# Kernel optimization log

Hardware: AMD Instinct MI355X
Metric: run time of the kernel (lower is better)

## Reference

```python
import jax, jax.numpy as jnp
import numpy as np

B, T, D, S, ITERS = 32, 4096, 256, 8, 3
SCALE = D ** -0.5
EPS = 1e-8


def _ln(x, g, b):
    mu = jnp.mean(x, axis=-1, keepdims=True)
    var = jnp.var(x, axis=-1, keepdims=True)
    return (x - mu) / jnp.sqrt(var + 1e-5) * g + b


def setup_inputs() -> dict:
    key = jax.random.key(0)
    ks = jax.random.split(key, 16)
    w = lambda k, shp, s=0.02: jax.random.normal(k, shp, jnp.float32) * s
    return {
        "inputs": jax.random.normal(ks[0], (B, T, D), jnp.float32),
        "slots_mu": w(ks[1], (1, 1, D), 0.1),
        "slots_logsigma": w(ks[2], (1, 1, D), 0.1),
        "noise": jax.random.normal(ks[3], (B, S, D), jnp.float32),
        "Wq": w(ks[4], (D, D)),
        "Wk": w(ks[5], (D, D)),
        "Wv": w(ks[6], (D, D)),
        "norm_g": jnp.ones((D,), jnp.float32),
        "norm_b": jnp.zeros((D,), jnp.float32),
        "gru_wih": w(ks[7], (D, 3 * D)),
        "gru_whh": w(ks[8], (D, 3 * D)),
        "gru_bih": jnp.zeros((3 * D,), jnp.float32),
        "gru_bhh": jnp.zeros((3 * D,), jnp.float32),
        "mlp_ng": jnp.ones((D,), jnp.float32),
        "mlp_nb": jnp.zeros((D,), jnp.float32),
        "mlp_w1": w(ks[9], (D, 4 * D)),
        "mlp_b1": jnp.zeros((4 * D,), jnp.float32),
        "mlp_w2": w(ks[10], (4 * D, D)),
        "mlp_b2": jnp.zeros((D,), jnp.float32),
    }


def reference(inputs, slots_mu, slots_logsigma, noise, Wq, Wk, Wv, norm_g, norm_b,
              gru_wih, gru_whh, gru_bih, gru_bhh, mlp_ng, mlp_nb,
              mlp_w1, mlp_b1, mlp_w2, mlp_b2):
    # init slots: mu + sigma * noise, broadcast [1,1,D] -> [B,S,D]
    slots = slots_mu + jnp.exp(slots_logsigma) * noise

    keys = inputs @ Wk      # [B,T,D]
    values = inputs @ Wv    # [B,T,D]

    for _ in range(ITERS):
        slots_prev = slots
        s_n = _ln(slots, norm_g, norm_b)
        q = s_n @ Wq                                    # [B,S,D]
        dots = jnp.einsum('bsd,btd->bst', q, keys) * SCALE
        attn = jax.nn.softmax(dots, axis=1) + EPS       # softmax over slots
        attn = attn / jnp.sum(attn, axis=-1, keepdims=True)
        updates = jnp.einsum('bst,btd->bsd', attn, values)

        # GRUCell: x = updates, h = slots_prev (elementwise over B*S)
        gi = updates @ gru_wih + gru_bih                # [B,S,3D]
        gh = slots_prev @ gru_whh + gru_bhh
        ir, iz, inn = jnp.split(gi, 3, axis=-1)
        hr, hz, hn = jnp.split(gh, 3, axis=-1)
        r = jax.nn.sigmoid(ir + hr)
        z = jax.nn.sigmoid(iz + hz)
        n = jnp.tanh(inn + r * hn)
        slots = (1.0 - z) * n + z * slots_prev

        # pre-norm residual MLP
        h = _ln(slots, mlp_ng, mlp_nb)
        h = jax.nn.relu(h @ mlp_w1 + mlp_b1)
        slots = slots + (h @ mlp_w2 + mlp_b2)

    return slots
```

## Files before the change

### kernel.cpp

```cpp
#include <hip/hip_runtime.h>
#include <stdint.h>

#define B_ 32
#define T_ 4096
#define D_ 256
#define S_ 8
#define ITERS_ 3
#define SCALE_ 0.0625f
#define EPS_ 1e-8f
#define NCH 16
#define CHUNK (T_/NCH)

typedef short short8 __attribute__((ext_vector_type(8)));
typedef float f32x4 __attribute__((ext_vector_type(4)));

__device__ __forceinline__ uint32_t f2bf1(float x){
  union { float f; uint32_t u; } c; c.f = x;
  return (c.u + 0x7fffu + ((c.u >> 16) & 1u)) >> 16;
}
__device__ __forceinline__ uint32_t pack2bf(float a, float b){
  return f2bf1(a) | (f2bf1(b) << 16);
}
__device__ __forceinline__ uint32_t cvtpk2bf(float a, float b){
  uint32_t r;
  asm("v_cvt_pk_bf16_f32 %0, %1, %2" : "=v"(r) : "v"(a), "v"(b));
  return r;
}
__device__ __forceinline__ float bflo(uint32_t u){ union{uint32_t u;float f;} c; c.u = u << 16; return c.f; }
__device__ __forceinline__ float bfhi(uint32_t u){ union{uint32_t u;float f;} c; c.u = u & 0xffff0000u; return c.f; }

__global__ __launch_bounds__(256) void k_prep(const float* __restrict__ Wk, const float* __restrict__ Wv,
                                              const float* __restrict__ Wq,
                                              const float* __restrict__ wih, const float* __restrict__ whh,
                                              const float* __restrict__ bih, const float* __restrict__ bhh,
                                              const float* __restrict__ w1, const float* __restrict__ w2,
                                              const float* __restrict__ mu, const float* __restrict__ ls,
                                              const float* __restrict__ noise,
                                              uint16_t* __restrict__ Wt, uint16_t* __restrict__ Wqt,
                                              uint16_t* __restrict__ Bcat, float* __restrict__ bc,
                                              uint16_t* __restrict__ w1t, uint16_t* __restrict__ w2t,
                                              float* __restrict__ slots){
  int g = blockIdx.x, tid = threadIdx.x;
  if (g < 512){
    int n = g, k = tid;
    float v = (n < 256) ? Wk[k*256 + n] : Wv[k*256 + (n - 256)];
    Wt[n*256 + k] = (uint16_t)f2bf1(v);
  } else if (g < 768){
    int n = g - 512, k = tid;
    Wqt[n*256 + k] = (uint16_t)f2bf1(Wq[k*256 + n] * SCALE_);
  } else if (g < 1792){
    int n = g - 768;
    #pragma unroll
    for (int j = 0; j < 2; ++j){
      int k = j*256 + tid;
      float v;
      if (n < 768) v = (k < 256) ? wih[k*768 + n] : whh[(k-256)*768 + n];
      else         v = (k < 256) ? 0.f            : whh[(k-256)*768 + 512 + (n-768)];
      Bcat[(size_t)n*512 + k] = (uint16_t)f2bf1(v);
    }
  } else if (g < 1793){
    #pragma unroll
    for (int j = 0; j < 4; ++j){
      int i = j*256 + tid;
      float v;
      if (i < 512) v = bih[i] + bhh[i];
      else if (i < 768) v = bih[i];
      else v = bhh[i - 256];
      bc[i] = v;
    }
  } else if (g < 2817){
    int n = g - 1793, k = tid;
    w1t[(size_t)n*256 + k] = (uint16_t)f2bf1(w1[(size_t)k*1024 + n]);
  } else if (g < 3073){
    int n = g - 2817;
    #pragma unroll
    for (int j = 0; j < 4; ++j){
      int k = j*256 + tid;
      w2t[(size_t)n*1024 + k] = (uint16_t)f2bf1(w2[(size_t)k*256 + n]);
    }
  } else {
    int i = (g - 3073)*256 + tid;
    int d = i & 255;
    slots[i] = mu[d] + __expf(ls[d]) * noise[i];
  }
}

#define PPITCH 40
__global__ __launch_bounds__(256) void k_proj(const float* __restrict__ X,
                                              const uint16_t* __restrict__ Wt,
                                              uint16_t* __restrict__ Kp,
                                              uint16_t* __restrict__ Vp){
  __shared__ __align__(16) uint16_t As[128*PPITCH];
  __shared__ __align__(16) uint16_t Bs[128*PPITCH];
  __shared__ __align__(16) uint16_t Cs[128*128];
  int bid = blockIdx.x;
  int x = bid & 7, j = bid >> 3;
  int tau = 512*x + j;
  int mt = tau >> 2;
  int nt = tau & 3;
  int m0 = mt * 128;
  int n0 = nt * 128;
  int tid = threadIdx.x;
  int lane = tid & 63, wid = tid >> 6;
  int wm = wid >> 1, wn = wid & 1;
  int rsel = lane & 15, g = lane >> 4;

  f32x4 acc[4][4];
  for (int a = 0; a < 4; ++a)
    for (int b = 0; b < 4; ++b)
      acc[a][b] = (f32x4){0.f,0.f,0.f,0.f};

  for (int ks = 0; ks < 8; ++ks){
    int k0 = ks*32;
    #pragma unroll
    for (int i = 0; i < 2; ++i){
      int task = i*256 + tid;
      int row = task >> 2, seg = task & 3;
      const float* gp = X + (size_t)(m0 + row)*256 + k0 + seg*8;
      float4 a = *(const float4*)gp;
      float4 b = *(const float4*)(gp + 4);
      uint4 w;
      w.x = cvtpk2bf(a.x, a.y); w.y = cvtpk2bf(a.z, a.w);
      w.z = cvtpk2bf(b.x, b.y); w.w = cvtpk2bf(b.z, b.w);
      *(uint4*)&As[row*PPITCH + seg*8] = w;
    }
    #pragma unroll
    for (int i = 0; i < 2; ++i){
      int task = i*256 + tid;
      int row = task >> 2, seg = task & 3;
      uint4 v = *(const uint4*)(Wt + (size_t)(n0 + row)*256 + k0 + seg*8);
      *(uint4*)&Bs[row*PPITCH + seg*8] = v;
    }
    __syncthreads();
    short8 af[4], bfr[4];
    #pragma unroll
    for (int t = 0; t < 4; ++t)
      af[t] = *(const short8*)&As[(wm*64 + t*16 + rsel)*PPITCH + g*8];
    #pragma unroll
    for (int t = 0; t < 4; ++t)
      bfr[t] = *(const short8*)&Bs[(wn*64 + t*16 + rsel)*PPITCH + g*8];
    #pragma unroll
    for (int a = 0; a < 4; ++a)
      #pragma unroll
      for (int b = 0; b < 4; ++b)
        acc[a][b] = __builtin_amdgcn_mfma_f32_16x16x32_bf16(af[a], bfr[b], acc[a][b], 0, 0, 0);
    __syncthreads();
  }
  #pragma unroll
  for (int a = 0; a < 4; ++a)
    #pragma unroll
    for (int b = 0; b < 4; ++b)
      #pragma unroll
      for (int r = 0; r < 4; ++r){
        int mrow = wm*64 + a*16 + g*4 + r;
        int ncol = wn*64 + b*16 + rsel;
        Cs[mrow*128 + ncol] = (uint16_t)f2bf1(acc[a][b][r]);
      }
  __syncthreads();
  uint16_t* outp = (n0 < 256) ? Kp : Vp;
  int nbase = n0 & 255;
  #pragma unroll
  for (int i = 0; i < 4; ++i){
    int task = i*256 + tid;
    int row = task >> 3, seg = task & 7;
    uint4 v = *(uint4*)&Cs[row*128 + seg*16];
    *(uint4*)&outp[(size_t)(m0 + row)*256 + nbase + seg*16] = v;
  }
}

__global__ __launch_bounds__(256) void k_qln(const float* __restrict__ slots,
                                             const uint16_t* __restrict__ Wqt,
                                             const float* __restrict__ ng,
                                             const float* __restrict__ nb,
                                             uint16_t* __restrict__ qbf){
  __shared__ __align__(16) uint16_t snl[16*264];
  int m0 = blockIdx.x * 16;
  int tid = threadIdx.x;
  int r = tid >> 4, cs = (tid & 15) * 16;
  float xv[16];
  {
    const float* sp = slots + (size_t)(m0 + r)*256 + cs;
    #pragma unroll
    for (int i = 0; i < 4; ++i){
      float4 v = *(const float4*)(sp + i*4);
      xv[i*4+0]=v.x; xv[i*4+1]=v.y; xv[i*4+2]=v.z; xv[i*4+3]=v.w;
    }
  }
  float s1 = 0.f, s2 = 0.f;
  #pragma unroll
  for (int i = 0; i < 16; ++i){ s1 += xv[i]; s2 += xv[i]*xv[i]; }
  #pragma unroll
  for (int m = 1; m < 16; m <<= 1){ s1 += __shfl_xor(s1, m, 64); s2 += __shfl_xor(s2, m, 64); }
  float mu = s1 * (1.f/256.f);
  float ms = s2 * (1.f/256.f);
  float rstd = rsqrtf(ms - mu*mu + 1e-5f);
  {
    uint32_t pk[8];
    #pragma unroll
    for (int i = 0; i < 8; ++i){
      float a = (xv[2*i]   - mu)*rstd*ng[cs+2*i]   + nb[cs+2*i];
      float b = (xv[2*i+1] - mu)*rstd*ng[cs+2*i+1] + nb[cs+2*i+1];
      pk[i] = pack2bf(a, b);
    }
    uint4* dst = (uint4*)&snl[r*264 + cs];
    dst[0] = (uint4){pk[0],pk[1],pk[2],pk[3]};
    dst[1] = (uint4){pk[4],pk[5],pk[6],pk[7]};
  }
  __syncthreads();
  int lane = tid & 63, w = tid >> 6;
  int rsel = lane & 15, g = lane >> 4;
  short8 aq[8];
  #pragma unroll
  for (int kk = 0; kk < 8; ++kk)
    aq[kk] = *(const short8*)((const char*)snl + rsel*528 + kk*64 + g*16);
  int n0w = w*64;
  #pragma unroll
  for (int nt = 0; nt < 4; ++nt){
    f32x4 acc = (f32x4){0.f,0.f,0.f,0.f};
    #pragma unroll
    for (int kk = 0; kk < 8; ++kk){
      short8 bfr = *(const short8*)&Wqt[(size_t)(n0w + nt*16 + rsel)*256 + kk*32 + g*8];
      acc = __builtin_amdgcn_mfma_f32_16x16x32_bf16(aq[kk], bfr, acc, 0, 0, 0);
    }
    #pragma unroll
    for (int r4 = 0; r4 < 4; ++r4){
      int row = g*4 + r4;
      qbf[(size_t)(m0 + row)*256 + n0w + nt*16 + rsel] = (uint16_t)f2bf1(acc[r4]);
    }
  }
}

#define GPIT 40
__global__ __launch_bounds__(256) void k_gemmG(const uint16_t* __restrict__ A,
                                               const uint16_t* __restrict__ Bm,
                                               float* __restrict__ Cf){
  __shared__ __align__(16) uint16_t As[64*GPIT];
  __shared__ __align__(16) uint16_t Bs[64*GPIT];
  const int N = 1024, K = 512;
  int m0 = blockIdx.y * 64, n0 = blockIdx.x * 64;
  int tid = threadIdx.x, lane = tid & 63, wid = tid >> 6;
  int wm = wid >> 1, wn = wid & 1;
  int rsel = lane & 15, g = lane >> 4;
  f32x4 acc[2][2];
  #pragma unroll
  for (int a = 0; a < 2; ++a)
    #pragma unroll
    for (int b = 0; b < 2; ++b)
      acc[a][b] = (f32x4){0.f,0.f,0.f,0.f};
  int row_s = tid >> 2, seg = tid & 3;
  for (int k0 = 0; k0 < K; k0 += 32){
    *(uint4*)&As[row_s*GPIT + seg*8] = *(const uint4*)(A  + (size_t)(m0+row_s)*K + k0 + seg*8);
    *(uint4*)&Bs[row_s*GPIT + seg*8] = *(const uint4*)(Bm + (size_t)(n0+row_s)*K + k0 + seg*8);
    __syncthreads();
    short8 af[2], bfr[2];
    #pragma unroll
    for (int t = 0; t < 2; ++t)
      af[t]  = *(const short8*)&As[(wm*32 + t*16 + rsel)*GPIT + g*8];
    #pragma unroll
    for (int t = 0; t < 2; ++t)
      bfr[t] = *(const short8*)&Bs[(wn*32 + t*16 + rsel)*GPIT + g*8];
    #pragma unroll
    for (int a = 0; a < 2; ++a)
      #pragma unroll
      for (int b = 0; b < 2; ++b)
        acc[a][b] = __builtin_amdgcn_mfma_f32_16x16x32_bf16(af[a], bfr[b], acc[a][b], 0, 0, 0);
    __syncthreads();
  }
  #pragma unroll
  for (int a = 0; a < 2; ++a)
    #pragma unroll
    for (int b = 0; b < 2; ++b)
      #pragma unroll
      for (int r = 0; r < 4; ++r){
        int mrow = m0 + wm*32 + a*16 + g*4 + r;
        int ncol = n0 + wn*32 + b*16 + rsel;
        Cf[(size_t)mrow*N + ncol] = acc[a][b][r];
      }
}

__global__ __launch_bounds__(256) void k_gru_pre(const float* __restrict__ upd_part,
                                                 const float* __restrict__ sum_part,
                                                 const float* __restrict__ slots,
                                                 uint16_t* __restrict__ Acat){
  int row = blockIdx.x;
  int b = row >> 3, s = row & 7;
  int d = threadIdx.x;
  float sum = 0.f;
  #pragma unroll
  for (int ch = 0; ch < 16; ++ch) sum += sum_part[(size_t)(b*16 + ch)*8 + s];
  float acc = 0.f;
  #pragma unroll
  for (int ch = 0; ch < 16; ++ch) acc += upd_part[(size_t)(b*16 + ch)*2048 + s*256 + d];
  Acat[(size_t)row*512 + d]       = (uint16_t)f2bf1(acc / sum);
  Acat[(size_t)row*512 + 256 + d] = (uint16_t)f2bf1(slots[row*256 + d]);
}

__global__ __launch_bounds__(256) void k_combine(const float* __restrict__ G,
                                                 const float* __restrict__ bc,
                                                 const float* __restrict__ slots,
                                                 const float* __restrict__ mng,
                                                 const float* __restrict__ mnb,
                                                 float* __restrict__ s2f,
                                                 uint16_t* __restrict__ snb){
  __shared__ float red[8];
  int row = blockIdx.x, c = threadIdx.x;
  int lane = c & 63, wid = c >> 6;
  const float* Gr = G + (size_t)row*1024;
  float r  = 1.f / (1.f + __expf(-(Gr[c]       + bc[c])));
  float z  = 1.f / (1.f + __expf(-(Gr[256 + c] + bc[256 + c])));
  float Gn = Gr[512 + c], Gh = Gr[768 + c];
  float nn = tanhf((Gn - Gh + bc[512 + c]) + r*(Gh + bc[768 + c]));
  float hv = slots[row*256 + c];
  float s2 = (1.f - z)*nn + z*hv;
  s2f[row*256 + c] = s2;
  float p1 = s2, p2 = s2*s2;
  #pragma unroll
  for (int d = 32; d; d >>= 1){ p1 += __shfl_down(p1, d, 64); p2 += __shfl_down(p2, d, 64); }
  if (lane == 0){ red[wid] = p1; red[4 + wid] = p2; }
  __syncthreads();
  float mu = (red[0]+red[1]+red[2]+red[3]) * (1.f/256.f);
  float ms = (red[4]+red[5]+red[6]+red[7]) * (1.f/256.f);
  float rstd = rsqrtf(ms - mu*mu + 1e-5f);
  snb[row*256 + c] = (uint16_t)f2bf1((s2 - mu)*rstd*mng[c] + mnb[c]);
}

#define HPIT 1048
__global__ __launch_bounds__(256) void k_mlp(const uint16_t* __restrict__ snb,
                                             const uint16_t* __restrict__ w1t,
                                             const float* __restrict__ b1,
                                             const uint16_t* __restrict__ w2t,
                                             const float* __restrict__ b2,
                                             const float* __restrict__ s2f,
                                             float* __restrict__ slots){
  __shared__ __align__(16) uint16_t h1s[16*HPIT];
  int m0 = blockIdx.x * 16;
  int tid = threadIdx.x, lane = tid & 63, w = tid >> 6;
  int rsel = lane & 15, g = lane >> 4;
  short8 aq[8];
  #pragma unroll
  for (int kk = 0; kk < 8; ++kk)
    aq[kk] = *(const short8*)&snb[(size_t)(m0 + rsel)*256 + kk*32 + g*8];
  #pragma unroll
  for (int nt = 0; nt < 16; ++nt){
    int ncol = w*256 + nt*16 + rsel;
    f32x4 acc = (f32x4){0.f,0.f,0.f,0.f};
    #pragma unroll
    for (int kk = 0; kk < 8; ++kk){
      short8 bfr = *(const short8*)&w1t[(size_t)ncol*256 + kk*32 + g*8];
      acc = __builtin_amdgcn_mfma_f32_16x16x32_bf16(aq[kk], bfr, acc, 0, 0, 0);
    }
    float bv = b1[ncol];
    #pragma unroll
    for (int r4 = 0; r4 < 4; ++r4){
      int row = g*4 + r4;
      h1s[row*HPIT + ncol] = (uint16_t)f2bf1(fmaxf(acc[r4] + bv, 0.f));
    }
  }
  __syncthreads();
  f32x4 acc2[4];
  #pragma unroll
  for (int nt = 0; nt < 4; ++nt) acc2[nt] = (f32x4){0.f,0.f,0.f,0.f};
  for (int kk = 0; kk < 32; ++kk){
    short8 aq2 = *(const short8*)((const char*)h1s + rsel*2096 + kk*64 + g*16);
    #pragma unroll
    for (int nt = 0; nt < 4; ++nt){
      short8 bfr = *(const short8*)&w2t[(size_t)(w*64 + nt*16 + rsel)*1024 + kk*32 + g*8];
      acc2[nt] = __builtin_amdgcn_mfma_f32_16x16x32_bf16(aq2, bfr, acc2[nt], 0, 0, 0);
    }
  }
  #pragma unroll
  for (int nt = 0; nt < 4; ++nt){
    int ncol = w*64 + nt*16 + rsel;
    float bv = b2[ncol];
    #pragma unroll
    for (int r4 = 0; r4 < 4; ++r4){
      int row = m0 + g*4 + r4;
      slots[(size_t)row*256 + ncol] = s2f[(size_t)row*256 + ncol] + acc2[nt][r4] + bv;
    }
  }
}

__global__ __launch_bounds__(256) void k_attn(const uint16_t* __restrict__ qbf,
                                              const uint16_t* __restrict__ Kp,
                                              const uint16_t* __restrict__ Vp,
                                              float* __restrict__ upd_part,
                                              float* __restrict__ sum_part){
  __shared__ __align__(16) uint16_t qs[16*264];
  __shared__ __align__(16) uint16_t Ks[64*264];
  __shared__ __align__(16) uint32_t attp[64*4];
  __shared__ float red[8*256];
  __shared__ float ssum[8];
  int bid = blockIdx.x;
  int b = bid >> 4, ch = bid & 15;
  int tid = threadIdx.x, lane = tid & 63, wid = tid >> 6;
  {
    const uint32_t* qg = (const uint32_t*)(qbf + (size_t)b*2048);
    uint32_t* qd = (uint32_t*)qs;
    #pragma unroll
    for (int i = 0; i < 4; ++i){
      int idx = i*256 + tid;
      int s = idx >> 7, c = idx & 127;
      qd[s*132 + c] = qg[idx];
    }
    #pragma unroll
    for (int i = 0; i < 5; ++i){
      int idx = i*256 + tid;
      if (idx < 1056) qd[8*132 + idx] = 0u;
    }
  }
  if (tid < 8) ssum[tid] = 0.f;
  __syncthreads();
  short8 aq[8];
  {
    int rs = lane & 15, g = lane >> 4;
    const char* qb = (const char*)qs;
    #pragma unroll
    for (int kk = 0; kk < 8; ++kk)
      aq[kk] = *(const short8*)(qb + rs*528 + kk*64 + g*16);
  }
  float upd[8][4];
  #pragma unroll
  for (int s = 0; s < 8; ++s){ upd[s][0]=0.f; upd[s][1]=0.f; upd[s][2]=0.f; upd[s][3]=0.f; }
  float sp[4] = {0.f,0.f,0.f,0.f};
  int dd = lane * 4;
  int tq = wid;

  for (int st = 0; st < 4; ++st){
    int t0 = ch*CHUNK + st*64;
    {
      const char* kg = (const char*)Kp + ((size_t)(b*T_ + t0) << 9);
      char* kd = (char*)Ks;
      #pragma unroll
      for (int i = 0; i < 8; ++i){
        int task = i*256 + tid;
        int row = task >> 5, seg = task & 31;
        uint4 v = *(const uint4*)(kg + (row << 9) + (seg << 4));
        *(uint4*)(kd + row*528 + seg*16) = v;
      }
    }
    __syncthreads();
    f32x4 dot = (f32x4){0.f,0.f,0.f,0.f};
    int col = lane & 15, g = lane >> 4;
    {
      const char* kb = (const char*)Ks + (wid*16 + col)*528 + g*16;
      #pragma unroll
      for (int kk = 0; kk < 8; ++kk){
        short8 bf = *(const short8*)(kb + kk*64);
        dot = __builtin_amdgcn_mfma_f32_16x16x32_bf16(aq[kk], bf, dot, 0, 0, 0);
      }
    }
    float x0 = dot[0], x1 = dot[1], x2 = dot[2], x3 = dot[3];
    float y0 = __shfl_xor(x0, 16, 64), y1 = __shfl_xor(x1, 16, 64);
    float y2 = __shfl_xor(x2, 16, 64), y3 = __shfl_xor(x3, 16, 64);
    float m = fmaxf(fmaxf(fmaxf(x0,x1), fmaxf(x2,x3)), fmaxf(fmaxf(y0,y1), fmaxf(y2,y3)));
    float e0 = __expf(x0-m), e1 = __expf(x1-m), e2 = __expf(x2-m), e3 = __expf(x3-m);
    float f0 = __expf(y0-m), f1 = __expf(y1-m), f2 = __expf(y2-m), f3 = __expf(y3-m);
    float inv = 1.f / (e0+e1+e2+e3+f0+f1+f2+f3);
    float p0 = e0*inv + EPS_, p1 = e1*inv + EPS_, p2 = e2*inv + EPS_, p3 = e3*inv + EPS_;
    if (g < 2){
      sp[0] += p0; sp[1] += p1; sp[2] += p2; sp[3] += p3;
      int t = wid*16 + col;
      attp[t*4 + g*2 + 0] = pack2bf(p0, p1);
      attp[t*4 + g*2 + 1] = pack2bf(p2, p3);
    }
    __syncthreads();
    {
      const char* vg = (const char*)Vp + ((size_t)(b*T_ + t0) << 9) + (size_t)dd*2;
      #pragma unroll
      for (int tt = 0; tt < 16; ++tt){
        int tl = tq*16 + tt;
        uint2 vv = *(const uint2*)(vg + ((size_t)tl << 9));
        uint4 aa = *(const uint4*)&attp[tl*4];
        float v0 = bflo(vv.x), v1 = bfhi(vv.x), v2 = bflo(vv.y), v3 = bfhi(vv.y);
        float av[8];
        av[0] = bflo(aa.x); av[1] = bfhi(aa.x); av[2] = bflo(aa.y); av[3] = bfhi(aa.y);
        av[4] = bflo(aa.z); av[5] = bfhi(aa.z); av[6] = bflo(aa.w); av[7] = bfhi(aa.w);
        #pragma unroll
        for (int s = 0; s < 8; ++s){
          upd[s][0] = fmaf(av[s], v0, upd[s][0]);
          upd[s][1] = fmaf(av[s], v1, upd[s][1]);
          upd[s][2] = fmaf(av[s], v2, upd[s][2]);
          upd[s][3] = fmaf(av[s], v3, upd[s][3]);
        }
      }
    }
    __syncthreads();
  }
  for (int ph = 0; ph < 4; ++ph){
    if (tq == ph){
      #pragma unroll
      for (int s = 0; s < 8; ++s)
        #pragma unroll
        for (int j2 = 0; j2 < 4; ++j2){
          if (ph == 0) red[s*256 + dd + j2]  = upd[s][j2];
          else         red[s*256 + dd + j2] += upd[s][j2];
        }
    }
    __syncthreads();
  }
  {
    float* up = upd_part + (size_t)bid * 2048;
    #pragma unroll
    for (int i = 0; i < 8; ++i) up[i*256 + tid] = red[i*256 + tid];
  }
  {
    int col = lane & 15, g = lane >> 4;
    #pragma unroll
    for (int dsh = 1; dsh < 16; dsh <<= 1){
      sp[0] += __shfl_xor(sp[0], dsh, 64); sp[1] += __shfl_xor(sp[1], dsh, 64);
      sp[2] += __shfl_xor(sp[2], dsh, 64); sp[3] += __shfl_xor(sp[3], dsh, 64);
    }
    if (col == 0 && g < 2){
      atomicAdd(&ssum[g*4 + 0], sp[0]);
      atomicAdd(&ssum[g*4 + 1], sp[1]);
      atomicAdd(&ssum[g*4 + 2], sp[2]);
      atomicAdd(&ssum[g*4 + 3], sp[3]);
    }
    __syncthreads();
    if (tid < 8) sum_part[(size_t)bid*8 + tid] = ssum[tid];
  }
}

extern "C" void kernel_launch(void* const* d_in, const int* in_sizes, int n_in,
                              void* d_out, int out_size, void* d_ws, size_t ws_size,
                              hipStream_t stream){
  const float* inputs = (const float*)d_in[0];
  const float* mu     = (const float*)d_in[1];
  const float* lsig   = (const float*)d_in[2];
  const float* noise  = (const float*)d_in[3];
  const float* Wq     = (const float*)d_in[4];
  const float* Wk     = (const float*)d_in[5];
  const float* Wv     = (const float*)d_in[6];
  const float* ng     = (const float*)d_in[7];
  const float* nb     = (const float*)d_in[8];
  const float* wih    = (const float*)d_in[9];
  const float* whh    = (const float*)d_in[10];
  const float* bih    = (const float*)d_in[11];
  const float* bhh    = (const float*)d_in[12];
  const float* mng    = (const float*)d_in[13];
  const float* mnb    = (const float*)d_in[14];
  const float* w1     = (const float*)d_in[15];
  const float* b1     = (const float*)d_in[16];
  const float* w2     = (const float*)d_in[17];
  const float* b2     = (const float*)d_in[18];
  float* slots = (float*)d_out;

  char* ws = (char*)d_ws;
  uint16_t* Wt       = (uint16_t*)(ws + 0);
  uint16_t* qbf      = (uint16_t*)(ws + 0x40000);
  float*    sum_part = (float*)   (ws + 0x60000);
  float*    upd_part = (float*)   (ws + 0x64000);
  uint16_t* Wqt      = (uint16_t*)(ws + 0x480000);
  uint16_t* Bcat     = (uint16_t*)(ws + 0x4A0000);
  uint16_t* w1t      = (uint16_t*)(ws + 0x5A0000);
  uint16_t* w2t      = (uint16_t*)(ws + 0x620000);
  float*    bc       = (float*)   (ws + 0x6A0000);
  uint16_t* Acat     = (uint16_t*)(ws + 0x6B0000);
  float*    G        = (float*)   (ws + 0x6F0000);
  uint16_t* snb      = (uint16_t*)(ws + 0x7F0000);
  float*    s2f      = (float*)   (ws + 0x810000);
  uint16_t* Kp       = (uint16_t*)(ws + 0x1000000);
  uint16_t* Vp       = (uint16_t*)(ws + 0x5000000);

  hipLaunchKernelGGL(k_prep, dim3(3329), dim3(256), 0, stream,
                     Wk, Wv, Wq, wih, whh, bih, bhh, w1, w2, mu, lsig, noise,
                     Wt, Wqt, Bcat, bc, w1t, w2t, slots);
  hipLaunchKernelGGL(k_proj, dim3(4096), dim3(256), 0, stream, inputs, Wt, Kp, Vp);

  for (int it = 0; it < ITERS_; ++it){
    hipLaunchKernelGGL(k_qln,     dim3(16),   dim3(256), 0, stream, slots, Wqt, ng, nb, qbf);
    hipLaunchKernelGGL(k_attn,    dim3(512),  dim3(256), 0, stream, qbf, Kp, Vp, upd_part, sum_part);
    hipLaunchKernelGGL(k_gru_pre, dim3(256),  dim3(256), 0, stream, upd_part, sum_part, slots, Acat);
    hipLaunchKernelGGL(k_gemmG,   dim3(16,4), dim3(256), 0, stream, Acat, Bcat, G);
    hipLaunchKernelGGL(k_combine, dim3(256),  dim3(256), 0, stream, G, bc, slots, mng, mnb, s2f, snb);
    hipLaunchKernelGGL(k_mlp,     dim3(16),   dim3(256), 0, stream, snb, w1t, b1, w2t, b2, s2f, slots);
  }
}
```

Measured before the change: 645.2 us.

## Fuse slot LN+Q projection into attention, split MLP into tiled GEMMs, restage k_proj

```diff
diff --git a/kernel.cpp b/kernel.cpp
--- a/kernel.cpp
+++ b/kernel.cpp
@@ -28,6 +28,12 @@
 }
 __device__ __forceinline__ float bflo(uint32_t u){ union{uint32_t u;float f;} c; c.u = u << 16; return c.f; }
 __device__ __forceinline__ float bfhi(uint32_t u){ union{uint32_t u;float f;} c; c.u = u & 0xffff0000u; return c.f; }
+
+__device__ __forceinline__ void gload16(const uint16_t* g, uint16_t* l){
+  __builtin_amdgcn_global_load_lds(
+      (const __attribute__((address_space(1))) uint32_t*)g,
+      (__attribute__((address_space(3))) uint32_t*)l, 16, 0, 0);
+}
 
 __global__ __launch_bounds__(256) void k_prep(const float* __restrict__ Wk, const float* __restrict__ Wv,
                                               const float* __restrict__ Wq,
@@ -85,159 +91,106 @@
   }
 }
 
-#define PPITCH 40
 __global__ __launch_bounds__(256) void k_proj(const float* __restrict__ X,
                                               const uint16_t* __restrict__ Wt,
                                               uint16_t* __restrict__ Kp,
                                               uint16_t* __restrict__ Vp){
-  __shared__ __align__(16) uint16_t As[128*PPITCH];
-  __shared__ __align__(16) uint16_t Bs[128*PPITCH];
-  __shared__ __align__(16) uint16_t Cs[128*128];
+  __shared__ __align__(16) uint16_t As[8192];
+  __shared__ __align__(16) uint16_t Bs[8192];
+  __shared__ __align__(16) uint16_t Cs[64*136];
   int bid = blockIdx.x;
   int x = bid & 7, j = bid >> 3;
   int tau = 512*x + j;
-  int mt = tau >> 2;
-  int nt = tau & 3;
-  int m0 = mt * 128;
-  int n0 = nt * 128;
+  int m0 = (tau >> 2) * 128;
+  int n0 = (tau & 3) * 128;
   int tid = threadIdx.x;
   int lane = tid & 63, wid = tid >> 6;
   int wm = wid >> 1, wn = wid & 1;
   int rsel = lane & 15, g = lane >> 4;
 
   f32x4 acc[4][4];
+  #pragma unroll
   for (int a = 0; a < 4; ++a)
+    #pragma unroll
     for (int b = 0; b < 4; ++b)
       acc[a][b] = (f32x4){0.f,0.f,0.f,0.f};
 
-  for (int ks = 0; ks < 8; ++ks){
-    int k0 = ks*32;
-    #pragma unroll
-    for (int i = 0; i < 2; ++i){
-      int task = i*256 + tid;
-      int row = task >> 2, seg = task & 3;
-      const float* gp = X + (size_t)(m0 + row)*256 + k0 + seg*8;
+  for (int ks = 0; ks < 4; ++ks){
+    int k0 = ks*64;
+    #pragma unroll
+    for (int i = 0; i < 4; ++i){
+      int c = wid*4 + i;
+      int T = c >> 1, kk = c & 1;
+      const uint16_t* src = Wt + (size_t)(n0 + T*16 + rsel)*256 + k0 + kk*32 + g*8;
+      gload16(src, &Bs[c*512]);
+    }
+    #pragma unroll
+    for (int i2 = 0; i2 < 4; ++i2){
+      int chunk = i2*256 + tid;
+      int blk = chunk >> 6, fl = chunk & 63;
+      int T = blk >> 1, kk = blk & 1;
+      const float* gp = X + (size_t)(m0 + T*16 + (fl & 15))*256 + k0 + kk*32 + (fl >> 4)*8;
       float4 a = *(const float4*)gp;
       float4 b = *(const float4*)(gp + 4);
       uint4 w;
       w.x = cvtpk2bf(a.x, a.y); w.y = cvtpk2bf(a.z, a.w);
       w.z = cvtpk2bf(b.x, b.y); w.w = cvtpk2bf(b.z, b.w);
-      *(uint4*)&As[row*PPITCH + seg*8] = w;
-    }
+      *(uint4*)&As[chunk*8] = w;
+    }
+    __syncthreads();
+    #pragma unroll
+    for (int kk = 0; kk < 2; ++kk){
+      short8 af[4], bfv[4];
+      #pragma unroll
+      for (int t = 0; t < 4; ++t)
+        af[t] = *(const short8*)&As[(((wm*4 + t) << 1) | kk)*512 + lane*8];
+      #pragma unroll
+      for (int t = 0; t < 4; ++t)
+        bfv[t] = *(const short8*)&Bs[(((wn*4 + t) << 1) | kk)*512 + lane*8];
+      #pragma unroll
+      for (int a = 0; a < 4; ++a)
+        #pragma unroll
+        for (int b = 0; b < 4; ++b)
+          acc[a][b] = __builtin_amdgcn_mfma_f32_16x16x32_bf16(af[a], bfv[b], acc[a][b], 0, 0, 0);
+    }
+    __syncthreads();
+  }
+  uint16_t* outp = (n0 < 256) ? Kp : Vp;
+  int nbase = n0 & 255;
+  for (int h = 0; h < 2; ++h){
+    if (wm == h){
+      #pragma unroll
+      for (int a = 0; a < 4; ++a)
+        #pragma unroll
+        for (int b = 0; b < 4; ++b)
+          #pragma unroll
+          for (int r = 0; r < 4; ++r)
+            Cs[(a*16 + g*4 + r)*136 + wn*64 + b*16 + rsel] = (uint16_t)f2bf1(acc[a][b][r]);
+    }
+    __syncthreads();
     #pragma unroll
     for (int i = 0; i < 2; ++i){
       int task = i*256 + tid;
-      int row = task >> 2, seg = task & 3;
-      uint4 v = *(const uint4*)(Wt + (size_t)(n0 + row)*256 + k0 + seg*8);
-      *(uint4*)&Bs[row*PPITCH + seg*8] = v;
-    }
-    __syncthreads();
-    short8 af[4], bfr[4];
-    #pragma unroll
-    for (int t = 0; t < 4; ++t)
-      af[t] = *(const short8*)&As[(wm*64 + t*16 + rsel)*PPITCH + g*8];
-    #pragma unroll
-    for (int t = 0; t < 4; ++t)
-      bfr[t] = *(const short8*)&Bs[(wn*64 + t*16 + rsel)*PPITCH + g*8];
-    #pragma unroll
-    for (int a = 0; a < 4; ++a)
-      #pragma unroll
-      for (int b = 0; b < 4; ++b)
-        acc[a][b] = __builtin_amdgcn_mfma_f32_16x16x32_bf16(af[a], bfr[b], acc[a][b], 0, 0, 0);
-    __syncthreads();
-  }
-  #pragma unroll
-  for (int a = 0; a < 4; ++a)
-    #pragma unroll
-    for (int b = 0; b < 4; ++b)
-      #pragma unroll
-      for (int r = 0; r < 4; ++r){
-        int mrow = wm*64 + a*16 + g*4 + r;
-        int ncol = wn*64 + b*16 + rsel;
-        Cs[mrow*128 + ncol] = (uint16_t)f2bf1(acc[a][b][r]);
-      }
-  __syncthreads();
-  uint16_t* outp = (n0 < 256) ? Kp : Vp;
-  int nbase = n0 & 255;
-  #pragma unroll
-  for (int i = 0; i < 4; ++i){
-    int task = i*256 + tid;
-    int row = task >> 3, seg = task & 7;
-    uint4 v = *(uint4*)&Cs[row*128 + seg*16];
-    *(uint4*)&outp[(size_t)(m0 + row)*256 + nbase + seg*16] = v;
-  }
-}
-
-__global__ __launch_bounds__(256) void k_qln(const float* __restrict__ slots,
-                                             const uint16_t* __restrict__ Wqt,
-                                             const float* __restrict__ ng,
-                                             const float* __restrict__ nb,
-                                             uint16_t* __restrict__ qbf){
-  __shared__ __align__(16) uint16_t snl[16*264];
-  int m0 = blockIdx.x * 16;
-  int tid = threadIdx.x;
-  int r = tid >> 4, cs = (tid & 15) * 16;
-  float xv[16];
-  {
-    const float* sp = slots + (size_t)(m0 + r)*256 + cs;
-    #pragma unroll
-    for (int i = 0; i < 4; ++i){
-      float4 v = *(const float4*)(sp + i*4);
-      xv[i*4+0]=v.x; xv[i*4+1]=v.y; xv[i*4+2]=v.z; xv[i*4+3]=v.w;
-    }
-  }
-  float s1 = 0.f, s2 = 0.f;
-  #pragma unroll
-  for (int i = 0; i < 16; ++i){ s1 += xv[i]; s2 += xv[i]*xv[i]; }
-  #pragma unroll
-  for (int m = 1; m < 16; m <<= 1){ s1 += __shfl_xor(s1, m, 64); s2 += __shfl_xor(s2, m, 64); }
-  float mu = s1 * (1.f/256.f);
-  float ms = s2 * (1.f/256.f);
-  float rstd = rsqrtf(ms - mu*mu + 1e-5f);
-  {
-    uint32_t pk[8];
-    #pragma unroll
-    for (int i = 0; i < 8; ++i){
-      float a = (xv[2*i]   - mu)*rstd*ng[cs+2*i]   + nb[cs+2*i];
-      float b = (xv[2*i+1] - mu)*rstd*ng[cs+2*i+1] + nb[cs+2*i+1];
-      pk[i] = pack2bf(a, b);
-    }
-    uint4* dst = (uint4*)&snl[r*264 + cs];
-    dst[0] = (uint4){pk[0],pk[1],pk[2],pk[3]};
-    dst[1] = (uint4){pk[4],pk[5],pk[6],pk[7]};
-  }
-  __syncthreads();
-  int lane = tid & 63, w = tid >> 6;
-  int rsel = lane & 15, g = lane >> 4;
-  short8 aq[8];
-  #pragma unroll
-  for (int kk = 0; kk < 8; ++kk)
-    aq[kk] = *(const short8*)((const char*)snl + rsel*528 + kk*64 + g*16);
-  int n0w = w*64;
-  #pragma unroll
-  for (int nt = 0; nt < 4; ++nt){
-    f32x4 acc = (f32x4){0.f,0.f,0.f,0.f};
-    #pragma unroll
-    for (int kk = 0; kk < 8; ++kk){
-      short8 bfr = *(const short8*)&Wqt[(size_t)(n0w + nt*16 + rsel)*256 + kk*32 + g*8];
-      acc = __builtin_amdgcn_mfma_f32_16x16x32_bf16(aq[kk], bfr, acc, 0, 0, 0);
-    }
-    #pragma unroll
-    for (int r4 = 0; r4 < 4; ++r4){
-      int row = g*4 + r4;
-      qbf[(size_t)(m0 + row)*256 + n0w + nt*16 + rsel] = (uint16_t)f2bf1(acc[r4]);
-    }
+      int row = task >> 3, seg = task & 7;
+      uint4 v = *(uint4*)&Cs[row*136 + seg*16];
+      *(uint4*)&outp[(size_t)(m0 + h*64 + row)*256 + nbase + seg*16] = v;
+    }
+    if (h == 0) __syncthreads();
   }
 }
 
 #define GPIT 40
-__global__ __launch_bounds__(256) void k_gemmG(const uint16_t* __restrict__ A,
-                                               const uint16_t* __restrict__ Bm,
-                                               float* __restrict__ Cf){
+template<int MODE>
+__global__ __launch_bounds__(256) void k_gemm64(const uint16_t* __restrict__ A,
+                                                const uint16_t* __restrict__ Bm,
+                                                const float* __restrict__ bias,
+                                                float* __restrict__ Cf,
+                                                uint16_t* __restrict__ Cb,
+                                                int N, int K, int kpb){
   __shared__ __align__(16) uint16_t As[64*GPIT];
   __shared__ __align__(16) uint16_t Bs[64*GPIT];
-  const int N = 1024, K = 512;
   int m0 = blockIdx.y * 64, n0 = blockIdx.x * 64;
+  int kb = blockIdx.z * kpb;
   int tid = threadIdx.x, lane = tid & 63, wid = tid >> 6;
   int wm = wid >> 1, wn = wid & 1;
   int rsel = lane & 15, g = lane >> 4;
@@ -248,7 +201,7 @@
     for (int b = 0; b < 2; ++b)
       acc[a][b] = (f32x4){0.f,0.f,0.f,0.f};
   int row_s = tid >> 2, seg = tid & 3;
-  for (int k0 = 0; k0 < K; k0 += 32){
+  for (int k0 = kb; k0 < kb + kpb; k0 += 32){
     *(uint4*)&As[row_s*GPIT + seg*8] = *(const uint4*)(A  + (size_t)(m0+row_s)*K + k0 + seg*8);
     *(uint4*)&Bs[row_s*GPIT + seg*8] = *(const uint4*)(Bm + (size_t)(n0+row_s)*K + k0 + seg*8);
     __syncthreads();
@@ -274,7 +227,10 @@
       for (int r = 0; r < 4; ++r){
         int mrow = m0 + wm*32 + a*16 + g*4 + r;
         int ncol = n0 + wn*32 + b*16 + rsel;
-        Cf[(size_t)mrow*N + ncol] = acc[a][b][r];
+        float v = acc[a][b][r];
+        if (MODE == 0) Cf[(size_t)mrow*N + ncol] = v;
+        if (MODE == 1) Cb[(size_t)mrow*N + ncol] = (uint16_t)f2bf1(fmaxf(v + bias[ncol], 0.f));
+        if (MODE == 4) atomicAdd(&Cf[(size_t)mrow*N + ncol], v);
       }
 }
 
@@ -297,10 +253,10 @@
 
 __global__ __launch_bounds__(256) void k_combine(const float* __restrict__ G,
                                                  const float* __restrict__ bc,
-                                                 const float* __restrict__ slots,
+                                                 float* __restrict__ slots,
                                                  const float* __restrict__ mng,
                                                  const float* __restrict__ mnb,
-                                                 float* __restrict__ s2f,
+                                                 const float* __restrict__ b2,
                                                  uint16_t* __restrict__ snb){
   __shared__ float red[8];
   int row = blockIdx.x, c = threadIdx.x;
@@ -312,7 +268,6 @@
   float nn = tanhf((Gn - Gh + bc[512 + c]) + r*(Gh + bc[768 + c]));
   float hv = slots[row*256 + c];
   float s2 = (1.f - z)*nn + z*hv;
-  s2f[row*256 + c] = s2;
   float p1 = s2, p2 = s2*s2;
   #pragma unroll
   for (int d = 32; d; d >>= 1){ p1 += __shfl_down(p1, d, 64); p2 += __shfl_down(p2, d, 64); }
@@ -322,65 +277,13 @@
   float ms = (red[4]+red[5]+red[6]+red[7]) * (1.f/256.f);
   float rstd = rsqrtf(ms - mu*mu + 1e-5f);
   snb[row*256 + c] = (uint16_t)f2bf1((s2 - mu)*rstd*mng[c] + mnb[c]);
-}
-
-#define HPIT 1048
-__global__ __launch_bounds__(256) void k_mlp(const uint16_t* __restrict__ snb,
-                                             const uint16_t* __restrict__ w1t,
-                                             const float* __restrict__ b1,
-                                             const uint16_t* __restrict__ w2t,
-                                             const float* __restrict__ b2,
-                                             const float* __restrict__ s2f,
-                                             float* __restrict__ slots){
-  __shared__ __align__(16) uint16_t h1s[16*HPIT];
-  int m0 = blockIdx.x * 16;
-  int tid = threadIdx.x, lane = tid & 63, w = tid >> 6;
-  int rsel = lane & 15, g = lane >> 4;
-  short8 aq[8];
-  #pragma unroll
-  for (int kk = 0; kk < 8; ++kk)
-    aq[kk] = *(const short8*)&snb[(size_t)(m0 + rsel)*256 + kk*32 + g*8];
-  #pragma unroll
-  for (int nt = 0; nt < 16; ++nt){
-    int ncol = w*256 + nt*16 + rsel;
-    f32x4 acc = (f32x4){0.f,0.f,0.f,0.f};
-    #pragma unroll
-    for (int kk = 0; kk < 8; ++kk){
-      short8 bfr = *(const short8*)&w1t[(size_t)ncol*256 + kk*32 + g*8];
-      acc = __builtin_amdgcn_mfma_f32_16x16x32_bf16(aq[kk], bfr, acc, 0, 0, 0);
-    }
-    float bv = b1[ncol];
-    #pragma unroll
-    for (int r4 = 0; r4 < 4; ++r4){
-      int row = g*4 + r4;
-      h1s[row*HPIT + ncol] = (uint16_t)f2bf1(fmaxf(acc[r4] + bv, 0.f));
-    }
-  }
-  __syncthreads();
-  f32x4 acc2[4];
-  #pragma unroll
-  for (int nt = 0; nt < 4; ++nt) acc2[nt] = (f32x4){0.f,0.f,0.f,0.f};
-  for (int kk = 0; kk < 32; ++kk){
-    short8 aq2 = *(const short8*)((const char*)h1s + rsel*2096 + kk*64 + g*16);
-    #pragma unroll
-    for (int nt = 0; nt < 4; ++nt){
-      short8 bfr = *(const short8*)&w2t[(size_t)(w*64 + nt*16 + rsel)*1024 + kk*32 + g*8];
-      acc2[nt] = __builtin_amdgcn_mfma_f32_16x16x32_bf16(aq2, bfr, acc2[nt], 0, 0, 0);
-    }
-  }
-  #pragma unroll
-  for (int nt = 0; nt < 4; ++nt){
-    int ncol = w*64 + nt*16 + rsel;
-    float bv = b2[ncol];
-    #pragma unroll
-    for (int r4 = 0; r4 < 4; ++r4){
-      int row = m0 + g*4 + r4;
-      slots[(size_t)row*256 + ncol] = s2f[(size_t)row*256 + ncol] + acc2[nt][r4] + bv;
-    }
-  }
-}
-
-__global__ __launch_bounds__(256) void k_attn(const uint16_t* __restrict__ qbf,
+  slots[row*256 + c] = s2 + b2[c];
+}
+
+__global__ __launch_bounds__(256) void k_attn(const float* __restrict__ slots,
+                                              const uint16_t* __restrict__ Wqt,
+                                              const float* __restrict__ ng,
+                                              const float* __restrict__ nb,
                                               const uint16_t* __restrict__ Kp,
                                               const uint16_t* __restrict__ Vp,
                                               float* __restrict__ upd_part,
@@ -388,35 +291,69 @@
   __shared__ __align__(16) uint16_t qs[16*264];
   __shared__ __align__(16) uint16_t Ks[64*264];
   __shared__ __align__(16) uint32_t attp[64*4];
-  __shared__ float red[8*256];
+  __shared__ union { uint16_t snl[16*264]; float red[8*256]; } u_;
   __shared__ float ssum[8];
   int bid = blockIdx.x;
   int b = bid >> 4, ch = bid & 15;
   int tid = threadIdx.x, lane = tid & 63, wid = tid >> 6;
+  int rsel = lane & 15, g = lane >> 4;
   {
-    const uint32_t* qg = (const uint32_t*)(qbf + (size_t)b*2048);
-    uint32_t* qd = (uint32_t*)qs;
+    int r = tid >> 5, h32 = tid & 31;
+    const float* sp = slots + (size_t)(b*8 + r)*256 + h32*8;
+    float4 v0 = *(const float4*)sp, v1 = *(const float4*)(sp + 4);
+    float xv[8] = {v0.x,v0.y,v0.z,v0.w,v1.x,v1.y,v1.z,v1.w};
+    float s1 = 0.f, s2 = 0.f;
+    #pragma unroll
+    for (int i = 0; i < 8; ++i){ s1 += xv[i]; s2 += xv[i]*xv[i]; }
+    #pragma unroll
+    for (int m = 1; m < 32; m <<= 1){ s1 += __shfl_xor(s1, m, 64); s2 += __shfl_xor(s2, m, 64); }
+    float mu = s1 * (1.f/256.f);
+    float ms = s2 * (1.f/256.f);
+    float rstd = rsqrtf(ms - mu*mu + 1e-5f);
+    const float* ngp = ng + h32*8; const float* nbp = nb + h32*8;
+    uint32_t pk[4];
     #pragma unroll
     for (int i = 0; i < 4; ++i){
-      int idx = i*256 + tid;
-      int s = idx >> 7, c = idx & 127;
-      qd[s*132 + c] = qg[idx];
-    }
+      float a = (xv[2*i]   - mu)*rstd*ngp[2*i]   + nbp[2*i];
+      float bb = (xv[2*i+1] - mu)*rstd*ngp[2*i+1] + nbp[2*i+1];
+      pk[i] = pack2bf(a, bb);
+    }
+    *(uint4*)&u_.snl[r*264 + h32*8] = (uint4){pk[0],pk[1],pk[2],pk[3]};
+    uint32_t* qd = (uint32_t*)u_.snl;
     #pragma unroll
     for (int i = 0; i < 5; ++i){
       int idx = i*256 + tid;
-      if (idx < 1056) qd[8*132 + idx] = 0u;
-    }
-  }
-  if (tid < 8) ssum[tid] = 0.f;
+      if (idx < 1056) qd[1056 + idx] = 0u;
+    }
+    if (tid < 8) ssum[tid] = 0.f;
+  }
+  __syncthreads();
+  {
+    short8 aqs[8];
+    #pragma unroll
+    for (int kk = 0; kk < 8; ++kk)
+      aqs[kk] = *(const short8*)((const char*)u_.snl + rsel*528 + kk*64 + g*16);
+    int n0w = wid*64;
+    #pragma unroll
+    for (int nt = 0; nt < 4; ++nt){
+      f32x4 acc = (f32x4){0.f,0.f,0.f,0.f};
+      #pragma unroll
+      for (int kk = 0; kk < 8; ++kk){
+        short8 bfr = *(const short8*)&Wqt[(size_t)(n0w + nt*16 + rsel)*256 + kk*32 + g*8];
+        acc = __builtin_amdgcn_mfma_f32_16x16x32_bf16(aqs[kk], bfr, acc, 0, 0, 0);
+      }
+      #pragma unroll
+      for (int r4 = 0; r4 < 4; ++r4)
+        qs[(g*4 + r4)*264 + n0w + nt*16 + rsel] = (uint16_t)f2bf1(acc[r4]);
+    }
+  }
   __syncthreads();
   short8 aq[8];
   {
-    int rs = lane & 15, g = lane >> 4;
     const char* qb = (const char*)qs;
     #pragma unroll
     for (int kk = 0; kk < 8; ++kk)
-      aq[kk] = *(const short8*)(qb + rs*528 + kk*64 + g*16);
+      aq[kk] = *(const short8*)(qb + rsel*528 + kk*64 + g*16);
   }
   float upd[8][4];
   #pragma unroll
@@ -440,9 +377,8 @@
     }
     __syncthreads();
     f32x4 dot = (f32x4){0.f,0.f,0.f,0.f};
-    int col = lane & 15, g = lane >> 4;
     {
-      const char* kb = (const char*)Ks + (wid*16 + col)*528 + g*16;
+      const char* kb = (const char*)Ks + (wid*16 + rsel)*528 + g*16;
       #pragma unroll
       for (int kk = 0; kk < 8; ++kk){
         short8 bf = *(const short8*)(kb + kk*64);
@@ -459,7 +395,7 @@
     float p0 = e0*inv + EPS_, p1 = e1*inv + EPS_, p2 = e2*inv + EPS_, p3 = e3*inv + EPS_;
     if (g < 2){
       sp[0] += p0; sp[1] += p1; sp[2] += p2; sp[3] += p3;
-      int t = wid*16 + col;
+      int t = wid*16 + rsel;
       attp[t*4 + g*2 + 0] = pack2bf(p0, p1);
       attp[t*4 + g*2 + 1] = pack2bf(p2, p3);
     }
@@ -492,8 +428,8 @@
       for (int s = 0; s < 8; ++s)
         #pragma unroll
         for (int j2 = 0; j2 < 4; ++j2){
-          if (ph == 0) red[s*256 + dd + j2]  = upd[s][j2];
-          else         red[s*256 + dd + j2] += upd[s][j2];
+          if (ph == 0) u_.red[s*256 + dd + j2]  = upd[s][j2];
+          else         u_.red[s*256 + dd + j2] += upd[s][j2];
         }
     }
     __syncthreads();
@@ -501,16 +437,15 @@
   {
     float* up = upd_part + (size_t)bid * 2048;
     #pragma unroll
-    for (int i = 0; i < 8; ++i) up[i*256 + tid] = red[i*256 + tid];
+    for (int i = 0; i < 8; ++i) up[i*256 + tid] = u_.red[i*256 + tid];
   }
   {
-    int col = lane & 15, g = lane >> 4;
     #pragma unroll
     for (int dsh = 1; dsh < 16; dsh <<= 1){
       sp[0] += __shfl_xor(sp[0], dsh, 64); sp[1] += __shfl_xor(sp[1], dsh, 64);
       sp[2] += __shfl_xor(sp[2], dsh, 64); sp[3] += __shfl_xor(sp[3], dsh, 64);
     }
-    if (col == 0 && g < 2){
+    if (rsel == 0 && g < 2){
       atomicAdd(&ssum[g*4 + 0], sp[0]);
       atomicAdd(&ssum[g*4 + 1], sp[1]);
       atomicAdd(&ssum[g*4 + 2], sp[2]);
@@ -547,7 +482,6 @@
 
   char* ws = (char*)d_ws;
   uint16_t* Wt       = (uint16_t*)(ws + 0);
-  uint16_t* qbf      = (uint16_t*)(ws + 0x40000);
   float*    sum_part = (float*)   (ws + 0x60000);
   float*    upd_part = (float*)   (ws + 0x64000);
   uint16_t* Wqt      = (uint16_t*)(ws + 0x480000);
@@ -558,7 +492,7 @@
   uint16_t* Acat     = (uint16_t*)(ws + 0x6B0000);
   float*    G        = (float*)   (ws + 0x6F0000);
   uint16_t* snb      = (uint16_t*)(ws + 0x7F0000);
-  float*    s2f      = (float*)   (ws + 0x810000);
+  uint16_t* h1b      = (uint16_t*)(ws + 0x850000);
   uint16_t* Kp       = (uint16_t*)(ws + 0x1000000);
   uint16_t* Vp       = (uint16_t*)(ws + 0x5000000);
 
@@ -568,11 +502,17 @@
   hipLaunchKernelGGL(k_proj, dim3(4096), dim3(256), 0, stream, inputs, Wt, Kp, Vp);
 
   for (int it = 0; it < ITERS_; ++it){
-    hipLaunchKernelGGL(k_qln,     dim3(16),   dim3(256), 0, stream, slots, Wqt, ng, nb, qbf);
-    hipLaunchKernelGGL(k_attn,    dim3(512),  dim3(256), 0, stream, qbf, Kp, Vp, upd_part, sum_part);
-    hipLaunchKernelGGL(k_gru_pre, dim3(256),  dim3(256), 0, stream, upd_part, sum_part, slots, Acat);
-    hipLaunchKernelGGL(k_gemmG,   dim3(16,4), dim3(256), 0, stream, Acat, Bcat, G);
-    hipLaunchKernelGGL(k_combine, dim3(256),  dim3(256), 0, stream, G, bc, slots, mng, mnb, s2f, snb);
-    hipLaunchKernelGGL(k_mlp,     dim3(16),   dim3(256), 0, stream, snb, w1t, b1, w2t, b2, s2f, slots);
-  }
-}
+    hipLaunchKernelGGL(k_attn,      dim3(512),    dim3(256), 0, stream,
+                       slots, Wqt, ng, nb, Kp, Vp, upd_part, sum_part);
+    hipLaunchKernelGGL(k_gru_pre,   dim3(256),    dim3(256), 0, stream,
+                       upd_part, sum_part, slots, Acat);
+    hipLaunchKernelGGL(k_gemm64<0>, dim3(16,4,1), dim3(256), 0, stream,
+                       Acat, Bcat, (const float*)nullptr, G, (uint16_t*)nullptr, 1024, 512, 512);
+    hipLaunchKernelGGL(k_combine,   dim3(256),    dim3(256), 0, stream,
+                       G, bc, slots, mng, mnb, b2, snb);
+    hipLaunchKernelGGL(k_gemm64<1>, dim3(16,4,1), dim3(256), 0, stream,
+                       snb, w1t, b1, (float*)nullptr, h1b, 1024, 256, 256);
+    hipLaunchKernelGGL(k_gemm64<4>, dim3(4,4,4),  dim3(256), 0, stream,
+                       h1b, w2t, (const float*)nullptr, slots, (uint16_t*)nullptr, 256, 1024, 256);
+  }
+}
```

Measured after the change: 516.2 us. -20.0%, faster.
